# Kernel optimization log

Measured on AMD Instinct MI355X. Metric: run time of the kernel, lower is better.

The kernel has to match this reference:

```python
import jax, jax.numpy as jnp
import numpy as np

N_NODES = 50000
N_EDGES = 800000
D_IN = 256
D_HID = 256
D_OUT = 256
BN_EPS = 1e-5
NORM_EPS = 1e-12


def _glorot(key, out_dim, in_dim):
    a = np.sqrt(6.0 / (in_dim + out_dim)).astype(np.float32)
    return jax.random.uniform(key, (out_dim, in_dim), jnp.float32, -a, a)


def setup_inputs() -> dict:
    key = jax.random.key(0)
    ks = jax.random.split(key, 8)
    x = jax.random.normal(ks[0], (N_NODES, D_IN), jnp.float32)
    edge_index = jax.random.randint(ks[1], (2, N_EDGES), 0, N_NODES, dtype=jnp.int32)
    batch = jnp.zeros((N_NODES,), jnp.int32)
    return {
        "x": x,
        "W1_l": _glorot(ks[2], D_HID, D_IN),
        "b1_l": jnp.zeros((D_HID,), jnp.float32),
        "W1_r": _glorot(ks[3], D_HID, D_IN),
        "W2_l": _glorot(ks[4], D_OUT, D_HID),
        "b2_l": jnp.zeros((D_OUT,), jnp.float32),
        "W2_r": _glorot(ks[5], D_OUT, D_HID),
        "gamma1": jnp.ones((D_HID,), jnp.float32),
        "beta1": jnp.zeros((D_HID,), jnp.float32),
        "edge_index": edge_index,
        "batch": batch,
    }


def _sage_conv(x, W_l, b_l, W_r, src, dst, n_nodes):
    # PyG SAGEConv (aggr='mean'): out = lin_l(mean_j x_j) + lin_r(x)
    msgs = x[src]                                            # [E, d] gather
    s = jax.ops.segment_sum(msgs, dst, num_segments=n_nodes)  # [N, d] scatter-add
    cnt = jax.ops.segment_sum(jnp.ones((src.shape[0], 1), x.dtype), dst,
                              num_segments=n_nodes)
    agg = jnp.where(cnt > 0, s / jnp.maximum(cnt, 1.0), 0.0)
    return agg @ W_l.T + b_l + x @ W_r.T


def _batch_norm(h, gamma, beta):
    mu = jnp.mean(h, axis=0)
    var = jnp.mean((h - mu) ** 2, axis=0)  # biased, as torch train-mode BN
    return (h - mu) * jax.lax.rsqrt(var + BN_EPS) * gamma + beta


def _l2_normalize(h):
    n = jnp.linalg.norm(h, axis=-1, keepdims=True)
    return h / jnp.maximum(n, NORM_EPS)


def reference(x, W1_l, b1_l, W1_r, W2_l, b2_l, W2_r, gamma1, beta1,
              edge_index, batch):
    n = x.shape[0]
    src, dst = edge_index[0], edge_index[1]
    # layer 1: SAGEConv -> BN (train stats) -> ReLU (dropout = identity in eval)
    h = _sage_conv(x, W1_l, b1_l, W1_r, src, dst, n)
    h = jax.nn.relu(_batch_norm(h, gamma1, beta1))
    # layer 2: SAGEConv -> L2 normalize
    h = _sage_conv(h, W2_l, b2_l, W2_r, src, dst, n)
    node_emb = _l2_normalize(h)
    # global mean pool over batch ids (single graph here), then normalize
    gsum = jax.ops.segment_sum(node_emb, batch, num_segments=1)
    gcnt = jax.ops.segment_sum(jnp.ones((n, 1), node_emb.dtype), batch,
                               num_segments=1)
    graph_emb = _l2_normalize(gsum / jnp.maximum(gcnt, 1.0))
    return node_emb, graph_emb
```

## Files before the change

### kernel.cpp

```cpp
#include <hip/hip_runtime.h>
#include <math.h>

#define NN 50000
#define NE 800000
#define D  256
#define SCB 196

typedef unsigned short u16;
typedef __attribute__((ext_vector_type(8))) short short8;
typedef __attribute__((ext_vector_type(8))) unsigned short u16x8;
typedef __attribute__((ext_vector_type(4))) float f32x4;

__device__ __forceinline__ u16 f2b(float f) {
    unsigned u = __float_as_uint(f);
    return (u16)((u + 0x7FFFu + ((u >> 16) & 1u)) >> 16);
}
__device__ __forceinline__ float b2f(u16 b) {
    return __uint_as_float(((unsigned)b) << 16);
}

__device__ __forceinline__ void gl16(const u16* g, u16* l) {
    __builtin_amdgcn_global_load_lds(
        (const __attribute__((address_space(1))) void*)g,
        (__attribute__((address_space(3))) void*)l, 16, 0, 0);
}

__global__ void degree_kernel(const int* __restrict__ dst, int* __restrict__ deg) {
    int e0 = (blockIdx.x * blockDim.x + threadIdx.x) * 4;
    if (e0 + 3 < NE) {
        int4 d = *(const int4*)&dst[e0];
        atomicAdd(&deg[d.x], 1);
        atomicAdd(&deg[d.y], 1);
        atomicAdd(&deg[d.z], 1);
        atomicAdd(&deg[d.w], 1);
    } else {
        for (int e = e0; e < NE; e++) atomicAdd(&deg[dst[e]], 1);
    }
}

__global__ void scanA_kernel(const int* __restrict__ deg, int* __restrict__ partial) {
    int t = threadIdx.x;
    int i = blockIdx.x * 256 + t;
    int v = (i < NN) ? deg[i] : 0;
#pragma unroll
    for (int o = 32; o; o >>= 1) v += __shfl_xor(v, o);
    __shared__ int sm[4];
    if ((t & 63) == 0) sm[t >> 6] = v;
    __syncthreads();
    if (t == 0) partial[blockIdx.x] = sm[0] + sm[1] + sm[2] + sm[3];
}

__global__ void scanB_kernel(const int* __restrict__ partial, int* __restrict__ base,
                             int* __restrict__ offs) {
    __shared__ int sm[256];
    int t = threadIdx.x;
    int v = (t < SCB) ? partial[t] : 0;
    sm[t] = v;
    __syncthreads();
    for (int off = 1; off < 256; off <<= 1) {
        int u = 0;
        if (t >= off) u = sm[t - off];
        __syncthreads();
        sm[t] += u;
        __syncthreads();
    }
    if (t < SCB) base[t] = sm[t] - v;
    if (t == 255) offs[NN] = sm[255];
}

__global__ void scanC_kernel(const int* __restrict__ deg, const int* __restrict__ base,
                             int* __restrict__ offs, int* __restrict__ cur) {
    __shared__ int sm[256];
    int t = threadIdx.x;
    int i = blockIdx.x * 256 + t;
    int v = (i < NN) ? deg[i] : 0;
    sm[t] = v;
    __syncthreads();
    for (int off = 1; off < 256; off <<= 1) {
        int u = 0;
        if (t >= off) u = sm[t - off];
        __syncthreads();
        sm[t] += u;
        __syncthreads();
    }
    int o = base[blockIdx.x] + sm[t] - v;
    if (i < NN) {
        offs[i] = o;
        cur[i] = o;
    }
}

__global__ void fill_kernel(const int* __restrict__ src, const int* __restrict__ dst,
                            int* __restrict__ cur, int* __restrict__ csr) {
    int e0 = (blockIdx.x * blockDim.x + threadIdx.x) * 4;
    if (e0 + 3 < NE) {
        int4 d = *(const int4*)&dst[e0];
        int4 s = *(const int4*)&src[e0];
        int p0 = atomicAdd(&cur[d.x], 1);
        int p1 = atomicAdd(&cur[d.y], 1);
        int p2 = atomicAdd(&cur[d.z], 1);
        int p3 = atomicAdd(&cur[d.w], 1);
        csr[p0] = s.x;
        csr[p1] = s.y;
        csr[p2] = s.z;
        csr[p3] = s.w;
    } else {
        for (int e = e0; e < NE; e++) {
            int pos = atomicAdd(&cur[dst[e]], 1);
            csr[pos] = src[e];
        }
    }
}

__global__ void wxconv_kernel(const float* __restrict__ x,
                              const float* __restrict__ W1l, const float* __restrict__ W1r,
                              const float* __restrict__ W2l, const float* __restrict__ W2r,
                              u16* __restrict__ Acat,
                              u16* __restrict__ Wcat1, u16* __restrict__ Wcat2) {
    int b = blockIdx.x;
    if (b < 12500) {
        int idx = b * 256 + threadIdx.x;
        int r = idx >> 6;
        int c4 = (idx & 63) * 4;
        float4 v = *(const float4*)&x[(size_t)r * 256 + c4];
        ushort4 o;
        o.x = f2b(v.x); o.y = f2b(v.y); o.z = f2b(v.z); o.w = f2b(v.w);
        *(ushort4*)&Acat[(size_t)r * 512 + 256 + c4] = o;
    } else {
        int r = b - 12500;
        int j = threadIdx.x;
        Wcat1[r * 512 + j]       = f2b(W1l[r * 256 + j]);
        Wcat1[r * 512 + 256 + j] = f2b(W1r[r * 256 + j]);
        Wcat2[r * 512 + j]       = f2b(W2l[r * 256 + j]);
        Wcat2[r * 512 + 256 + j] = f2b(W2r[r * 256 + j]);
    }
}

__global__ __launch_bounds__(256)
void agg_kernel(const u16* __restrict__ Acat, const int* __restrict__ csr,
                const int* __restrict__ offs, u16* __restrict__ AcatW) {
    int wid = (blockIdx.x * blockDim.x + threadIdx.x) >> 6;
    int lane = threadIdx.x & 63;
    if (wid >= NN) return;
    int beg = offs[wid];
    int end = offs[wid + 1];
    int deg = end - beg;
    int half = lane >> 5;
    int lc = (lane & 31) * 8;
    int mid = beg + ((deg + 1) >> 1);
    int e  = half ? mid : beg;
    int hi = half ? end : mid;
    float a[8] = {0.f, 0.f, 0.f, 0.f, 0.f, 0.f, 0.f, 0.f};
    for (; e + 7 < hi; e += 8) {
        int s0 = csr[e + 0], s1 = csr[e + 1], s2 = csr[e + 2], s3 = csr[e + 3];
        int s4 = csr[e + 4], s5 = csr[e + 5], s6 = csr[e + 6], s7 = csr[e + 7];
        u16x8 v0 = *(const u16x8*)&Acat[(size_t)s0 * 512 + 256 + lc];
        u16x8 v1 = *(const u16x8*)&Acat[(size_t)s1 * 512 + 256 + lc];
        u16x8 v2 = *(const u16x8*)&Acat[(size_t)s2 * 512 + 256 + lc];
        u16x8 v3 = *(const u16x8*)&Acat[(size_t)s3 * 512 + 256 + lc];
        u16x8 v4 = *(const u16x8*)&Acat[(size_t)s4 * 512 + 256 + lc];
        u16x8 v5 = *(const u16x8*)&Acat[(size_t)s5 * 512 + 256 + lc];
        u16x8 v6 = *(const u16x8*)&Acat[(size_t)s6 * 512 + 256 + lc];
        u16x8 v7 = *(const u16x8*)&Acat[(size_t)s7 * 512 + 256 + lc];
#pragma unroll
        for (int i = 0; i < 8; i++)
            a[i] += ((b2f(v0[i]) + b2f(v1[i])) + (b2f(v2[i]) + b2f(v3[i]))) +
                    ((b2f(v4[i]) + b2f(v5[i])) + (b2f(v6[i]) + b2f(v7[i])));
    }
    for (; e + 3 < hi; e += 4) {
        int s0 = csr[e + 0], s1 = csr[e + 1], s2 = csr[e + 2], s3 = csr[e + 3];
        u16x8 v0 = *(const u16x8*)&Acat[(size_t)s0 * 512 + 256 + lc];
        u16x8 v1 = *(const u16x8*)&Acat[(size_t)s1 * 512 + 256 + lc];
        u16x8 v2 = *(const u16x8*)&Acat[(size_t)s2 * 512 + 256 + lc];
        u16x8 v3 = *(const u16x8*)&Acat[(size_t)s3 * 512 + 256 + lc];
#pragma unroll
        for (int i = 0; i < 8; i++)
            a[i] += (b2f(v0[i]) + b2f(v1[i])) + (b2f(v2[i]) + b2f(v3[i]));
    }
    for (; e < hi; e++) {
        int s0 = csr[e];
        u16x8 v0 = *(const u16x8*)&Acat[(size_t)s0 * 512 + 256 + lc];
#pragma unroll
        for (int i = 0; i < 8; i++) a[i] += b2f(v0[i]);
    }
#pragma unroll
    for (int i = 0; i < 8; i++) a[i] += __shfl_xor(a[i], 32);
    float sc = (deg > 0) ? 1.0f / (float)deg : 0.0f;
    if (half == 0) {
        u16x8 o;
#pragma unroll
        for (int i = 0; i < 8; i++) o[i] = f2b(a[i] * sc);
        *(u16x8*)&AcatW[(size_t)wid * 512 + lc] = o;
    }
}

template<int BF16_OUT>
__global__ __launch_bounds__(256)
void mfma_gemm_kernel(const u16* __restrict__ A, const u16* __restrict__ W,
                      const float* __restrict__ bias, void* __restrict__ Cout) {
    __shared__ u16 S[4][2][2][64 * 32];
    const int tid = threadIdx.x;
    const int l = tid & 63;
    const int wid = tid >> 6;
    const int wr = wid >> 1, wc = wid & 1;
    const int row0 = blockIdx.x * 128;
    const int col0 = blockIdx.y * 128;

    const u16* aptr[4];
    const u16* bptr[4];
#pragma unroll
    for (int i = 0; i < 4; i++) {
        int rl = i * 16 + (l >> 2);
        int kg = (l & 3) ^ ((rl >> 1) & 3);
        int ra = row0 + wr * 64 + rl;
        if (ra > NN - 1) ra = NN - 1;
        aptr[i] = A + (size_t)ra * 512 + kg * 8;
        bptr[i] = W + (size_t)(col0 + wc * 64 + rl) * 512 + kg * 8;
    }

    f32x4 acc[4][4] = {};

#define STAGE(b, t)                                                     \
    do {                                                                \
        _Pragma("unroll") for (int i_ = 0; i_ < 4; i_++) {              \
            gl16(aptr[i_] + (t) * 32, &S[wid][b][0][i_ * 16 * 32]);     \
            gl16(bptr[i_] + (t) * 32, &S[wid][b][1][i_ * 16 * 32]);     \
        }                                                               \
    } while (0)

    STAGE(0, 0);

    const int kq = l >> 4;
    const int sw = ((l & 15) >> 1) & 3;
    const int slot = (kq ^ sw) * 8;
#pragma unroll
    for (int t = 0; t < 16; t++) {
        if (t < 15) {
            STAGE((t + 1) & 1, t + 1);
            asm volatile("s_waitcnt vmcnt(8)" ::: "memory");
        } else {
            asm volatile("s_waitcnt vmcnt(0)" ::: "memory");
        }
        __builtin_amdgcn_sched_barrier(0);

        const u16* As = &S[wid][t & 1][0][0];
        const u16* Bs = &S[wid][t & 1][1][0];
        short8 af[4], bf[4];
#pragma unroll
        for (int m = 0; m < 4; m++)
            af[m] = *(const short8*)&As[(m * 16 + (l & 15)) * 32 + slot];
#pragma unroll
        for (int n = 0; n < 4; n++)
            bf[n] = *(const short8*)&Bs[(n * 16 + (l & 15)) * 32 + slot];
#pragma unroll
        for (int m = 0; m < 4; m++)
#pragma unroll
            for (int n = 0; n < 4; n++)
                acc[m][n] = __builtin_amdgcn_mfma_f32_16x16x32_bf16(
                    af[m], bf[n], acc[m][n], 0, 0, 0);
    }
#undef STAGE

    const int cq = l >> 4;
    const int cc = l & 15;
#pragma unroll
    for (int m = 0; m < 4; m++) {
#pragma unroll
        for (int n = 0; n < 4; n++) {
            int c = col0 + wc * 64 + n * 16 + cc;
#pragma unroll
            for (int j = 0; j < 4; j++) {
                int r = row0 + wr * 64 + m * 16 + cq * 4 + j;
                if (r < NN) {
                    float v = acc[m][n][j] + bias[c];
                    if (BF16_OUT)
                        ((u16*)Cout)[(size_t)r * 256 + c] = f2b(v);
                    else
                        ((float*)Cout)[(size_t)r * 256 + c] = v;
                }
            }
        }
    }
}

__global__ void colstats_kernel(const u16* __restrict__ h, float* __restrict__ stats) {
    int j = threadIdx.x;
    float s0 = 0.f, s1 = 0.f;
    for (int r = blockIdx.x; r < NN; r += gridDim.x) {
        float v = b2f(h[(size_t)r * 256 + j]);
        s0 += v;
        s1 += v * v;
    }
    atomicAdd(&stats[j], s0);
    atomicAdd(&stats[256 + j], s1);
}

__global__ void bnrelu_kernel(const u16* __restrict__ hb,
                              const float* __restrict__ stats,
                              const float* __restrict__ gamma,
                              const float* __restrict__ beta,
                              u16* __restrict__ Acat) {
    __shared__ float s_scale[256], s_shift[256];
    int t = threadIdx.x;
    {
        const float invN = 1.0f / (float)NN;
        float mu = stats[t] * invN;
        float var = stats[256 + t] * invN - mu * mu;
        float sc = gamma[t] * rsqrtf(var + 1e-5f);
        s_scale[t] = sc;
        s_shift[t] = beta[t] - mu * sc;
    }
    __syncthreads();
    int idx = blockIdx.x * 256 + t;
    int r = idx >> 5;
    int c8 = (idx & 31) * 8;
    u16x8 v = *(const u16x8*)&hb[(size_t)r * 256 + c8];
    u16x8 o;
#pragma unroll
    for (int i = 0; i < 8; i++) {
        float f = b2f(v[i]) * s_scale[c8 + i] + s_shift[c8 + i];
        o[i] = f2b(fmaxf(f, 0.f));
    }
    *(u16x8*)&Acat[(size_t)r * 512 + 256 + c8] = o;
}

__global__ __launch_bounds__(512)
void l2norm_kernel(float* __restrict__ out, float* __restrict__ gsum) {
    __shared__ float sm[8 * 256];
    int wave = threadIdx.x >> 6;
    int lane = threadIdx.x & 63;
    float c0 = 0.f, c1 = 0.f, c2 = 0.f, c3 = 0.f;
    for (int r = blockIdx.x * 8 + wave; r < NN; r += gridDim.x * 8) {
        float4 v = *(float4*)&out[(size_t)r * 256 + lane * 4];
        float sq = v.x * v.x + v.y * v.y + v.z * v.z + v.w * v.w;
#pragma unroll
        for (int o = 32; o; o >>= 1) sq += __shfl_xor(sq, o);
        float invn = 1.0f / fmaxf(sqrtf(sq), 1e-12f);
        v.x *= invn; v.y *= invn; v.z *= invn; v.w *= invn;
        *(float4*)&out[(size_t)r * 256 + lane * 4] = v;
        c0 += v.x; c1 += v.y; c2 += v.z; c3 += v.w;
    }
    *(float4*)&sm[wave * 256 + lane * 4] = make_float4(c0, c1, c2, c3);
    __syncthreads();
    int t = threadIdx.x;
    if (t < 256) {
        float s = 0.f;
#pragma unroll
        for (int w = 0; w < 8; w++) s += sm[w * 256 + t];
        atomicAdd(&gsum[t], s);
    }
}

__global__ void graph_kernel(const float* __restrict__ gsum, float* __restrict__ gout) {
    __shared__ float wsum[4];
    int j = threadIdx.x;
    float v = gsum[j] * (1.0f / (float)NN);
    float sq = v * v;
#pragma unroll
    for (int o = 32; o; o >>= 1) sq += __shfl_xor(sq, o);
    if ((j & 63) == 0) wsum[j >> 6] = sq;
    __syncthreads();
    float tot = wsum[0] + wsum[1] + wsum[2] + wsum[3];
    gout[j] = v / fmaxf(sqrtf(tot), 1e-12f);
}

extern "C" void kernel_launch(void* const* d_in, const int* in_sizes, int n_in,
                              void* d_out, int out_size, void* d_ws, size_t ws_size,
                              hipStream_t stream) {
    const float* x      = (const float*)d_in[0];
    const float* W1_l   = (const float*)d_in[1];
    const float* b1_l   = (const float*)d_in[2];
    const float* W1_r   = (const float*)d_in[3];
    const float* W2_l   = (const float*)d_in[4];
    const float* b2_l   = (const float*)d_in[5];
    const float* W2_r   = (const float*)d_in[6];
    const float* gamma1 = (const float*)d_in[7];
    const float* beta1  = (const float*)d_in[8];
    const int*   eidx   = (const int*)d_in[9];
    const int* src = eidx;
    const int* dst = eidx + NE;

    char* wsb = (char*)d_ws;
    int*   deg   = (int*)(wsb + 0);
    int*   offs  = (int*)(wsb + 200000);
    int*   cur   = (int*)(wsb + 400004);
    int*   csr   = (int*)(wsb + 600004);
    int*   part  = (int*)(wsb + 3800064);
    int*   base  = (int*)(wsb + 3801088);
    float* stats = (float*)(wsb + 3802112);
    float* gsum  = (float*)(wsb + 3804160);
    u16*   Wcat1 = (u16*)(wsb + 3807232);
    u16*   Wcat2 = (u16*)(wsb + 4069376);
    u16*   hb    = (u16*)(wsb + 4331520);
    u16*   Acat  = (u16*)(wsb + 29931520);
    float* out   = (float*)d_out;
    float* gout  = out + (size_t)NN * 256;

    hipMemsetAsync(deg, 0, NN * sizeof(int), stream);
    hipMemsetAsync(stats, 0, 3072, stream);

    wxconv_kernel<<<12756, 256, 0, stream>>>(x, W1_l, W1_r, W2_l, W2_r,
                                             Acat, Wcat1, Wcat2);

    degree_kernel<<<(NE / 4 + 255) / 256, 256, 0, stream>>>(dst, deg);
    scanA_kernel<<<SCB, 256, 0, stream>>>(deg, part);
    scanB_kernel<<<1, 256, 0, stream>>>(part, base, offs);
    scanC_kernel<<<SCB, 256, 0, stream>>>(deg, base, offs, cur);
    fill_kernel<<<(NE / 4 + 255) / 256, 256, 0, stream>>>(src, dst, cur, csr);

    dim3 ggrid((NN + 127) / 128, 2);

    agg_kernel<<<12500, 256, 0, stream>>>(Acat, csr, offs, Acat);
    mfma_gemm_kernel<1><<<ggrid, 256, 0, stream>>>(Acat, Wcat1, b1_l, hb);
    colstats_kernel<<<512, 256, 0, stream>>>(hb, stats);
    bnrelu_kernel<<<6250, 256, 0, stream>>>(hb, stats, gamma1, beta1, Acat);

    agg_kernel<<<12500, 256, 0, stream>>>(Acat, csr, offs, Acat);
    mfma_gemm_kernel<0><<<ggrid, 256, 0, stream>>>(Acat, Wcat2, b2_l, out);

    l2norm_kernel<<<1024, 512, 0, stream>>>(out, gsum);
    graph_kernel<<<1, 256, 0, stream>>>(gsum, gout);
}
```

Before: 400.7 us.

## Fuse degree count into conversion kernel, widen fill, share GEMM LDS tiles

The degree-counting pass now runs as extra blocks of the input conversion kernel, which removes one kernel launch. The CSR fill kernel handles eight edges per thread instead of four. The GEMM now keeps a block-wide shared A/B tile in a 4-deep LDS ring that all waves load cooperatively and read with a barrier, prefetching two stages ahead. Before, each wave held private 64-row copies with double buffering, so the change cuts redundant global loads, at the cost of a block barrier every K step.

```diff
diff --git a/kernel.cpp b/kernel.cpp
--- a/kernel.cpp
+++ b/kernel.cpp
@@ -25,98 +25,13 @@
         (__attribute__((address_space(3))) void*)l, 16, 0, 0);
 }
 
-__global__ void degree_kernel(const int* __restrict__ dst, int* __restrict__ deg) {
-    int e0 = (blockIdx.x * blockDim.x + threadIdx.x) * 4;
-    if (e0 + 3 < NE) {
-        int4 d = *(const int4*)&dst[e0];
-        atomicAdd(&deg[d.x], 1);
-        atomicAdd(&deg[d.y], 1);
-        atomicAdd(&deg[d.z], 1);
-        atomicAdd(&deg[d.w], 1);
-    } else {
-        for (int e = e0; e < NE; e++) atomicAdd(&deg[dst[e]], 1);
-    }
-}
-
-__global__ void scanA_kernel(const int* __restrict__ deg, int* __restrict__ partial) {
-    int t = threadIdx.x;
-    int i = blockIdx.x * 256 + t;
-    int v = (i < NN) ? deg[i] : 0;
-#pragma unroll
-    for (int o = 32; o; o >>= 1) v += __shfl_xor(v, o);
-    __shared__ int sm[4];
-    if ((t & 63) == 0) sm[t >> 6] = v;
-    __syncthreads();
-    if (t == 0) partial[blockIdx.x] = sm[0] + sm[1] + sm[2] + sm[3];
-}
-
-__global__ void scanB_kernel(const int* __restrict__ partial, int* __restrict__ base,
-                             int* __restrict__ offs) {
-    __shared__ int sm[256];
-    int t = threadIdx.x;
-    int v = (t < SCB) ? partial[t] : 0;
-    sm[t] = v;
-    __syncthreads();
-    for (int off = 1; off < 256; off <<= 1) {
-        int u = 0;
-        if (t >= off) u = sm[t - off];
-        __syncthreads();
-        sm[t] += u;
-        __syncthreads();
-    }
-    if (t < SCB) base[t] = sm[t] - v;
-    if (t == 255) offs[NN] = sm[255];
-}
-
-__global__ void scanC_kernel(const int* __restrict__ deg, const int* __restrict__ base,
-                             int* __restrict__ offs, int* __restrict__ cur) {
-    __shared__ int sm[256];
-    int t = threadIdx.x;
-    int i = blockIdx.x * 256 + t;
-    int v = (i < NN) ? deg[i] : 0;
-    sm[t] = v;
-    __syncthreads();
-    for (int off = 1; off < 256; off <<= 1) {
-        int u = 0;
-        if (t >= off) u = sm[t - off];
-        __syncthreads();
-        sm[t] += u;
-        __syncthreads();
-    }
-    int o = base[blockIdx.x] + sm[t] - v;
-    if (i < NN) {
-        offs[i] = o;
-        cur[i] = o;
-    }
-}
-
-__global__ void fill_kernel(const int* __restrict__ src, const int* __restrict__ dst,
-                            int* __restrict__ cur, int* __restrict__ csr) {
-    int e0 = (blockIdx.x * blockDim.x + threadIdx.x) * 4;
-    if (e0 + 3 < NE) {
-        int4 d = *(const int4*)&dst[e0];
-        int4 s = *(const int4*)&src[e0];
-        int p0 = atomicAdd(&cur[d.x], 1);
-        int p1 = atomicAdd(&cur[d.y], 1);
-        int p2 = atomicAdd(&cur[d.z], 1);
-        int p3 = atomicAdd(&cur[d.w], 1);
-        csr[p0] = s.x;
-        csr[p1] = s.y;
-        csr[p2] = s.z;
-        csr[p3] = s.w;
-    } else {
-        for (int e = e0; e < NE; e++) {
-            int pos = atomicAdd(&cur[dst[e]], 1);
-            csr[pos] = src[e];
-        }
-    }
-}
-
 __global__ void wxconv_kernel(const float* __restrict__ x,
                               const float* __restrict__ W1l, const float* __restrict__ W1r,
                               const float* __restrict__ W2l, const float* __restrict__ W2r,
+                              const int* __restrict__ dst,
                               u16* __restrict__ Acat,
-                              u16* __restrict__ Wcat1, u16* __restrict__ Wcat2) {
+                              u16* __restrict__ Wcat1, u16* __restrict__ Wcat2,
+                              int* __restrict__ deg) {
     int b = blockIdx.x;
     if (b < 12500) {
         int idx = b * 256 + threadIdx.x;
@@ -126,13 +41,102 @@
         ushort4 o;
         o.x = f2b(v.x); o.y = f2b(v.y); o.z = f2b(v.z); o.w = f2b(v.w);
         *(ushort4*)&Acat[(size_t)r * 512 + 256 + c4] = o;
-    } else {
+    } else if (b < 12756) {
         int r = b - 12500;
         int j = threadIdx.x;
         Wcat1[r * 512 + j]       = f2b(W1l[r * 256 + j]);
         Wcat1[r * 512 + 256 + j] = f2b(W1r[r * 256 + j]);
         Wcat2[r * 512 + j]       = f2b(W2l[r * 256 + j]);
         Wcat2[r * 512 + 256 + j] = f2b(W2r[r * 256 + j]);
+    } else {
+        int e0 = ((b - 12756) * 256 + threadIdx.x) * 4;
+        if (e0 + 3 < NE) {
+            int4 d = *(const int4*)&dst[e0];
+            atomicAdd(&deg[d.x], 1);
+            atomicAdd(&deg[d.y], 1);
+            atomicAdd(&deg[d.z], 1);
+            atomicAdd(&deg[d.w], 1);
+        } else {
+            for (int e = e0; e < NE; e++) atomicAdd(&deg[dst[e]], 1);
+        }
+    }
+}
+
+__global__ void scanA_kernel(const int* __restrict__ deg, int* __restrict__ partial) {
+    int t = threadIdx.x;
+    int i = blockIdx.x * 256 + t;
+    int v = (i < NN) ? deg[i] : 0;
+#pragma unroll
+    for (int o = 32; o; o >>= 1) v += __shfl_xor(v, o);
+    __shared__ int sm[4];
+    if ((t & 63) == 0) sm[t >> 6] = v;
+    __syncthreads();
+    if (t == 0) partial[blockIdx.x] = sm[0] + sm[1] + sm[2] + sm[3];
+}
+
+__global__ void scanB_kernel(const int* __restrict__ partial, int* __restrict__ base,
+                             int* __restrict__ offs) {
+    __shared__ int sm[256];
+    int t = threadIdx.x;
+    int v = (t < SCB) ? partial[t] : 0;
+    sm[t] = v;
+    __syncthreads();
+    for (int off = 1; off < 256; off <<= 1) {
+        int u = 0;
+        if (t >= off) u = sm[t - off];
+        __syncthreads();
+        sm[t] += u;
+        __syncthreads();
+    }
+    if (t < SCB) base[t] = sm[t] - v;
+    if (t == 255) offs[NN] = sm[255];
+}
+
+__global__ void scanC_kernel(const int* __restrict__ deg, const int* __restrict__ base,
+                             int* __restrict__ offs, int* __restrict__ cur) {
+    __shared__ int sm[256];
+    int t = threadIdx.x;
+    int i = blockIdx.x * 256 + t;
+    int v = (i < NN) ? deg[i] : 0;
+    sm[t] = v;
+    __syncthreads();
+    for (int off = 1; off < 256; off <<= 1) {
+        int u = 0;
+        if (t >= off) u = sm[t - off];
+        __syncthreads();
+        sm[t] += u;
+        __syncthreads();
+    }
+    int o = base[blockIdx.x] + sm[t] - v;
+    if (i < NN) {
+        offs[i] = o;
+        cur[i] = o;
+    }
+}
+
+__global__ void fill_kernel(const int* __restrict__ src, const int* __restrict__ dst,
+                            int* __restrict__ cur, int* __restrict__ csr) {
+    int e0 = (blockIdx.x * blockDim.x + threadIdx.x) * 8;
+    if (e0 + 7 < NE) {
+        int4 d0 = *(const int4*)&dst[e0];
+        int4 d1 = *(const int4*)&dst[e0 + 4];
+        int4 s0 = *(const int4*)&src[e0];
+        int4 s1 = *(const int4*)&src[e0 + 4];
+        int p0 = atomicAdd(&cur[d0.x], 1);
+        int p1 = atomicAdd(&cur[d0.y], 1);
+        int p2 = atomicAdd(&cur[d0.z], 1);
+        int p3 = atomicAdd(&cur[d0.w], 1);
+        int p4 = atomicAdd(&cur[d1.x], 1);
+        int p5 = atomicAdd(&cur[d1.y], 1);
+        int p6 = atomicAdd(&cur[d1.z], 1);
+        int p7 = atomicAdd(&cur[d1.w], 1);
+        csr[p0] = s0.x; csr[p1] = s0.y; csr[p2] = s0.z; csr[p3] = s0.w;
+        csr[p4] = s1.x; csr[p5] = s1.y; csr[p6] = s1.z; csr[p7] = s1.w;
+    } else {
+        for (int e = e0; e < NE; e++) {
+            int pos = atomicAdd(&cur[dst[e]], 1);
+            csr[pos] = src[e];
+        }
     }
 }
 
@@ -198,7 +202,8 @@
 __global__ __launch_bounds__(256)
 void mfma_gemm_kernel(const u16* __restrict__ A, const u16* __restrict__ W,
                       const float* __restrict__ bias, void* __restrict__ Cout) {
-    __shared__ u16 S[4][2][2][64 * 32];
+    __shared__ u16 As[4][128 * 32];
+    __shared__ u16 Bs[4][128 * 32];
     const int tid = threadIdx.x;
     const int l = tid & 63;
     const int wid = tid >> 6;
@@ -206,52 +211,56 @@
     const int row0 = blockIdx.x * 128;
     const int col0 = blockIdx.y * 128;
 
-    const u16* aptr[4];
-    const u16* bptr[4];
-#pragma unroll
-    for (int i = 0; i < 4; i++) {
-        int rl = i * 16 + (l >> 2);
-        int kg = (l & 3) ^ ((rl >> 1) & 3);
-        int ra = row0 + wr * 64 + rl;
+    const u16* aptr[2];
+    const u16* bptr[2];
+#pragma unroll
+    for (int i = 0; i < 2; i++) {
+        int row = wid * 32 + i * 16 + (l >> 2);
+        int kg = (l & 3) ^ ((row >> 1) & 3);
+        int ra = row0 + row;
         if (ra > NN - 1) ra = NN - 1;
         aptr[i] = A + (size_t)ra * 512 + kg * 8;
-        bptr[i] = W + (size_t)(col0 + wc * 64 + rl) * 512 + kg * 8;
+        bptr[i] = W + (size_t)(col0 + row) * 512 + kg * 8;
     }
 
     f32x4 acc[4][4] = {};
 
-#define STAGE(b, t)                                                     \
-    do {                                                                \
-        _Pragma("unroll") for (int i_ = 0; i_ < 4; i_++) {              \
-            gl16(aptr[i_] + (t) * 32, &S[wid][b][0][i_ * 16 * 32]);     \
-            gl16(bptr[i_] + (t) * 32, &S[wid][b][1][i_ * 16 * 32]);     \
-        }                                                               \
+#define STAGE(b, t)                                                          \
+    do {                                                                     \
+        _Pragma("unroll") for (int i_ = 0; i_ < 2; i_++) {                   \
+            u16* al = &As[b][(wid * 32 + i_ * 16) * 32];                     \
+            u16* bl = &Bs[b][(wid * 32 + i_ * 16) * 32];                     \
+            gl16(aptr[i_] + (t) * 32, al);                                   \
+            gl16(bptr[i_] + (t) * 32, bl);                                   \
+        }                                                                    \
     } while (0)
 
     STAGE(0, 0);
+    STAGE(1, 1);
 
     const int kq = l >> 4;
     const int sw = ((l & 15) >> 1) & 3;
-    const int slot = (kq ^ sw) * 8;
 #pragma unroll
     for (int t = 0; t < 16; t++) {
-        if (t < 15) {
-            STAGE((t + 1) & 1, t + 1);
-            asm volatile("s_waitcnt vmcnt(8)" ::: "memory");
-        } else {
-            asm volatile("s_waitcnt vmcnt(0)" ::: "memory");
+        if (t + 2 < 16) STAGE((t + 2) & 3, t + 2);
+
+        if (t < 14)       asm volatile("s_waitcnt vmcnt(8)" ::: "memory");
+        else if (t == 14) asm volatile("s_waitcnt vmcnt(4)" ::: "memory");
+        else              asm volatile("s_waitcnt vmcnt(0)" ::: "memory");
+        __builtin_amdgcn_s_barrier();
+        __builtin_amdgcn_sched_barrier(0);
+
+        short8 af[4], bf[4];
+#pragma unroll
+        for (int m = 0; m < 4; m++) {
+            int row = wr * 64 + m * 16 + (l & 15);
+            af[m] = *(const short8*)&As[t & 3][row * 32 + (kq ^ sw) * 8];
         }
-        __builtin_amdgcn_sched_barrier(0);
-
-        const u16* As = &S[wid][t & 1][0][0];
-        const u16* Bs = &S[wid][t & 1][1][0];
-        short8 af[4], bf[4];
-#pragma unroll
-        for (int m = 0; m < 4; m++)
-            af[m] = *(const short8*)&As[(m * 16 + (l & 15)) * 32 + slot];
-#pragma unroll
-        for (int n = 0; n < 4; n++)
-            bf[n] = *(const short8*)&Bs[(n * 16 + (l & 15)) * 32 + slot];
+#pragma unroll
+        for (int n = 0; n < 4; n++) {
+            int row = wc * 64 + n * 16 + (l & 15);
+            bf[n] = *(const short8*)&Bs[t & 3][row * 32 + (kq ^ sw) * 8];
+        }
 #pragma unroll
         for (int m = 0; m < 4; m++)
 #pragma unroll
@@ -399,14 +408,14 @@
     hipMemsetAsync(deg, 0, NN * sizeof(int), stream);
     hipMemsetAsync(stats, 0, 3072, stream);
 
-    wxconv_kernel<<<12756, 256, 0, stream>>>(x, W1_l, W1_r, W2_l, W2_r,
-                                             Acat, Wcat1, Wcat2);
-
-    degree_kernel<<<(NE / 4 + 255) / 256, 256, 0, stream>>>(dst, deg);
+    const int DEGB = (NE / 4 + 255) / 256;
+    wxconv_kernel<<<12756 + DEGB, 256, 0, stream>>>(x, W1_l, W1_r, W2_l, W2_r,
+                                                    dst, Acat, Wcat1, Wcat2, deg);
+
     scanA_kernel<<<SCB, 256, 0, stream>>>(deg, part);
     scanB_kernel<<<1, 256, 0, stream>>>(part, base, offs);
     scanC_kernel<<<SCB, 256, 0, stream>>>(deg, base, offs, cur);
-    fill_kernel<<<(NE / 4 + 255) / 256, 256, 0, stream>>>(src, dst, cur, csr);
+    fill_kernel<<<(NE / 8 + 255) / 256, 256, 0, stream>>>(src, dst, cur, csr);
 
     dim3 ggrid((NN + 127) / 128, 2);
 
```

Result: faster. 387.4 us (-3.3%).
